# Kernel optimization log

Measured on AMD Instinct MI355X. Metric: run time of the kernel, lower is better.

Reference implementation:

```python
import jax, jax.numpy as jnp
import numpy as np

N = 100000
E = 1600000
IN_DIM = 128
OUT_DIM = 128


def setup_inputs() -> dict:
    key = jax.random.key(0)
    k1, k2, k3, k4, k5 = jax.random.split(key, 5)
    x = jax.random.normal(k1, (N, IN_DIM), dtype=jnp.float32)
    edge_index = jax.random.randint(k2, (2, E), 0, N, dtype=jnp.int64)
    # LayerNorm affine params
    ln_w = jnp.ones((IN_DIM,), dtype=jnp.float32)
    ln_b = jnp.zeros((IN_DIM,), dtype=jnp.float32)
    # SAGEConv params: lin_l (neighbor agg, with bias), lin_r (root, no bias)
    s = 1.0 / np.sqrt(IN_DIM)
    W_l = jax.random.uniform(k3, (OUT_DIM, IN_DIM), dtype=jnp.float32, minval=-s, maxval=s)
    b_l = jax.random.uniform(k4, (OUT_DIM,), dtype=jnp.float32, minval=-s, maxval=s)
    W_r = jax.random.uniform(k5, (OUT_DIM, IN_DIM), dtype=jnp.float32, minval=-s, maxval=s)
    return {"x": x, "edge_index": edge_index, "ln_w": ln_w, "ln_b": ln_b,
            "W_l": W_l, "b_l": b_l, "W_r": W_r}


def _layer_norm(x, w, b, eps=1e-5):
    mu = jnp.mean(x, axis=-1, keepdims=True)
    var = jnp.mean(jnp.square(x - mu), axis=-1, keepdims=True)
    return (x - mu) * jax.lax.rsqrt(var + eps) * w + b


def reference(x, edge_index, ln_w, ln_b, W_l, b_l, W_r):
    # norm -> activation -> dropout(p=0, identity)
    h = jax.nn.relu(_layer_norm(x, ln_w, ln_b))  # [N, in_dim]
    src = edge_index[0]  # message sources (x_j)
    dst = edge_index[1]  # aggregation targets
    # mean aggregation of neighbor features onto target nodes
    agg = jax.ops.segment_sum(h[src], dst, num_segments=N)  # [N, in_dim]
    cnt = jax.ops.segment_sum(jnp.ones((E,), dtype=h.dtype), dst, num_segments=N)
    agg = agg / jnp.maximum(cnt, 1.0)[:, None]
    # SAGEConv: lin_l(agg) + lin_r(h)
    out = agg @ W_l.T + b_l + h @ W_r.T  # [N, out_dim]
    return out
```

## Files before the change

kernel.cpp:

```cpp
#include <hip/hip_runtime.h>

#define N_NODES 100000
#define E_EDGES 1600000
#define DIM     128

#define NB1     196
#define CHUNK   8192
#define NBINS   512
#define NBUCKET 391
#define NBH     (NBINS * NB1)
#define HS_BLOCKS 98

#define HB_OFF    0
#define WTB_OFF   25600000
#define OFFS_OFF  25665536
#define BH_OFF    26065600
#define BSUM_OFF  26467008
#define BIN_OFF   26468032
#define SRC_OFF   32868032

typedef __attribute__((ext_vector_type(8))) short short8;
typedef __attribute__((ext_vector_type(4))) float floatx4;

__device__ __forceinline__ unsigned bf16pack(float a, float b) {
  unsigned ua = __float_as_uint(a); ua += 0x7fffu + ((ua >> 16) & 1u);
  unsigned ub = __float_as_uint(b); ub += 0x7fffu + ((ub >> 16) & 1u);
  return (ua >> 16) | (ub & 0xffff0000u);
}
__device__ __forceinline__ float2 bf16unpack(unsigned p) {
  return make_float2(__uint_as_float(p << 16), __uint_as_float(p & 0xffff0000u));
}

__global__ __launch_bounds__(256) void k_prep(const float* __restrict__ x,
                                              const float* __restrict__ lw,
                                              const float* __restrict__ lb,
                                              const float* __restrict__ Wl,
                                              const float* __restrict__ Wr,
                                              const int* __restrict__ ei,
                                              unsigned* __restrict__ hb,
                                              unsigned* __restrict__ wtb,
                                              int* __restrict__ bh) {
  int gid = blockIdx.x * 256 + threadIdx.x;
  int t = threadIdx.x;

  {
    int row  = blockIdx.x * 4 + (t >> 6);
    int lane = t & 63;
    float2 v = ((const float2*)(x + (size_t)row * DIM))[lane];
    float s  = v.x + v.y;
    float sq = v.x * v.x + v.y * v.y;
    #pragma unroll
    for (int off = 32; off > 0; off >>= 1) {
      s  += __shfl_xor(s, off);
      sq += __shfl_xor(sq, off);
    }
    float mu  = s * (1.0f / 128.0f);
    float var = sq * (1.0f / 128.0f) - mu * mu;
    float rs  = rsqrtf(var + 1e-5f);
    float2 w = ((const float2*)lw)[lane];
    float2 b = ((const float2*)lb)[lane];
    float ox = fmaxf((v.x - mu) * rs * w.x + b.x, 0.0f);
    float oy = fmaxf((v.y - mu) * rs * w.y + b.y, 0.0f);
    hb[(size_t)row * 64 + lane] = bf16pack(ox, oy);
  }

  if (gid < 16384) {
    int j2 = gid & 3;
    int q  = (gid >> 2) & 3;
    int c  = (gid >> 4) & 127;
    int kb = gid >> 11;
    int k0 = kb * 32 + q * 8 + j2 * 2;
    int k1 = k0 + 1;
    float v0 = (k0 < 128) ? Wl[c * 128 + k0] : Wr[c * 128 + (k0 - 128)];
    float v1 = (k1 < 128) ? Wl[c * 128 + k1] : Wr[c * 128 + (k1 - 128)];
    wtb[gid] = bf16pack(v0, v1);
  }

  if (blockIdx.x < NB1) {
    __shared__ int h[NBINS];
    h[t] = 0; h[t + 256] = 0;
    __syncthreads();
    const int4* d4p = (const int4*)(ei + E_EDGES);
    #pragma unroll
    for (int u = 0; u < 8; ++u) {
      int i4 = blockIdx.x * (CHUNK / 4) + u * 256 + t;
      if (i4 < E_EDGES / 4) {
        int4 d = d4p[i4];
        atomicAdd(&h[d.x >> 8], 1);
        atomicAdd(&h[d.y >> 8], 1);
        atomicAdd(&h[d.z >> 8], 1);
        atomicAdd(&h[d.w >> 8], 1);
      }
    }
    __syncthreads();
    bh[t * NB1 + blockIdx.x] = h[t];
    bh[(t + 256) * NB1 + blockIdx.x] = h[t + 256];
  }
}

__global__ __launch_bounds__(256) void k_hscan1(int* __restrict__ bh,
                                                int* __restrict__ bsum) {
  __shared__ int s[256];
  int t = threadIdx.x;
  int base = blockIdx.x * 1024 + t * 4;
  int a0 = (base + 0 < NBH) ? bh[base + 0] : 0;
  int a1 = (base + 1 < NBH) ? bh[base + 1] : 0;
  int a2 = (base + 2 < NBH) ? bh[base + 2] : 0;
  int a3 = (base + 3 < NBH) ? bh[base + 3] : 0;
  s[t] = a0 + a1 + a2 + a3;
  __syncthreads();
  #pragma unroll
  for (int off = 1; off < 256; off <<= 1) {
    int x = (t >= off) ? s[t - off] : 0;
    __syncthreads();
    s[t] += x;
    __syncthreads();
  }
  int excl = (t > 0) ? s[t - 1] : 0;
  if (t == 255) bsum[blockIdx.x] = s[255];
  if (base + 0 < NBH) bh[base + 0] = excl;
  if (base + 1 < NBH) bh[base + 1] = excl + a0;
  if (base + 2 < NBH) bh[base + 2] = excl + a0 + a1;
  if (base + 3 < NBH) bh[base + 3] = excl + a0 + a1 + a2;
}

__global__ __launch_bounds__(256) void k_binsort(const int* __restrict__ ei,
                                                 const int* __restrict__ bh,
                                                 const int* __restrict__ bsum,
                                                 int* __restrict__ binned) {
  __shared__ int stage[CHUNK];
  __shared__ int addr[CHUNK];
  __shared__ int hist[NBINS];
  __shared__ int ebase[NBINS];
  __shared__ int cur[NBINS];
  __shared__ int gbase[NBINS];
  __shared__ int s[256];
  __shared__ int bsc[256];
  int t  = threadIdx.x;
  int ch = blockIdx.x;

  s[t] = (t < HS_BLOCKS) ? bsum[t] : 0;
  __syncthreads();
  #pragma unroll
  for (int off = 1; off < 256; off <<= 1) {
    int xv = (t >= off) ? s[t - off] : 0;
    __syncthreads();
    s[t] += xv;
    __syncthreads();
  }
  bsc[t] = (t > 0) ? s[t - 1] : 0;
  __syncthreads();

  {
    int i0 = t * NB1 + ch;
    int i1 = (t + 256) * NB1 + ch;
    gbase[t]       = bh[i0] + bsc[i0 >> 10];
    gbase[t + 256] = bh[i1] + bsc[i1 >> 10];
  }
  hist[t] = 0; hist[t + 256] = 0;
  __syncthreads();

  const int4* s4p = (const int4*)ei;
  const int4* d4p = (const int4*)(ei + E_EDGES);

  #pragma unroll
  for (int u = 0; u < 8; ++u) {
    int i4 = ch * (CHUNK / 4) + u * 256 + t;
    if (i4 < E_EDGES / 4) {
      int4 d = d4p[i4];
      atomicAdd(&hist[d.x >> 8], 1);
      atomicAdd(&hist[d.y >> 8], 1);
      atomicAdd(&hist[d.z >> 8], 1);
      atomicAdd(&hist[d.w >> 8], 1);
    }
  }
  __syncthreads();

  int h0 = hist[2 * t], h1 = hist[2 * t + 1];
  s[t] = h0 + h1;
  __syncthreads();
  #pragma unroll
  for (int off = 1; off < 256; off <<= 1) {
    int xv = (t >= off) ? s[t - off] : 0;
    __syncthreads();
    s[t] += xv;
    __syncthreads();
  }
  int ex = (t > 0) ? s[t - 1] : 0;
  ebase[2 * t] = ex;
  ebase[2 * t + 1] = ex + h0;
  cur[2 * t] = ex;
  cur[2 * t + 1] = ex + h0;
  __syncthreads();

  #pragma unroll
  for (int u = 0; u < 8; ++u) {
    int i4 = ch * (CHUNK / 4) + u * 256 + t;
    if (i4 < E_EDGES / 4) {
      int4 sv = s4p[i4];
      int4 dv = d4p[i4];
      {
        int bin = dv.x >> 8; int pos = atomicAdd(&cur[bin], 1);
        stage[pos] = sv.x | ((dv.x & 255) << 20);
        addr[pos]  = gbase[bin] + (pos - ebase[bin]);
      }
      {
        int bin = dv.y >> 8; int pos = atomicAdd(&cur[bin], 1);
        stage[pos] = sv.y | ((dv.y & 255) << 20);
        addr[pos]  = gbase[bin] + (pos - ebase[bin]);
      }
      {
        int bin = dv.z >> 8; int pos = atomicAdd(&cur[bin], 1);
        stage[pos] = sv.z | ((dv.z & 255) << 20);
        addr[pos]  = gbase[bin] + (pos - ebase[bin]);
      }
      {
        int bin = dv.w >> 8; int pos = atomicAdd(&cur[bin], 1);
        stage[pos] = sv.w | ((dv.w & 255) << 20);
        addr[pos]  = gbase[bin] + (pos - ebase[bin]);
      }
    }
  }
  __syncthreads();

  int cbase = ch * CHUNK;
  int cnt = E_EDGES - cbase;
  if (cnt > CHUNK) cnt = CHUNK;
  for (int i = t; i < cnt; i += 256)
    binned[addr[i]] = stage[i];
}

__global__ __launch_bounds__(256) void k_csr(const int* __restrict__ bh,
                                             const int* __restrict__ bsum,
                                             const int* __restrict__ binned,
                                             int* __restrict__ offs,
                                             int* __restrict__ srcidx) {
  __shared__ int h[256];
  __shared__ int s[256];
  __shared__ int cur[256];
  __shared__ int bsc[256];
  int t = threadIdx.x;
  int bin = blockIdx.x;

  s[t] = (t < HS_BLOCKS) ? bsum[t] : 0;
  __syncthreads();
  #pragma unroll
  for (int off = 1; off < 256; off <<= 1) {
    int xv = (t >= off) ? s[t - off] : 0;
    __syncthreads();
    s[t] += xv;
    __syncthreads();
  }
  bsc[t] = (t > 0) ? s[t - 1] : 0;
  __syncthreads();

  int i0 = bin * NB1, i1 = (bin + 1) * NB1;
  int base = bh[i0] + bsc[i0 >> 10];
  int end  = bh[i1] + bsc[i1 >> 10];

  h[t] = 0;
  __syncthreads();
  for (int i = base + t; i < end; i += 256)
    atomicAdd(&h[(binned[i] >> 20) & 255], 1);
  __syncthreads();
  s[t] = h[t];
  __syncthreads();
  #pragma unroll
  for (int off = 1; off < 256; off <<= 1) {
    int x = (t >= off) ? s[t - off] : 0;
    __syncthreads();
    s[t] += x;
    __syncthreads();
  }
  int excl = (t > 0) ? s[t - 1] : 0;
  cur[t] = excl;
  int node = bin * 256 + t;
  if (node < N_NODES) offs[node] = base + excl;
  if (node == N_NODES) offs[N_NODES] = E_EDGES;
  __syncthreads();
  for (int i = base + t; i < end; i += 256) {
    int p = binned[i];
    int r = atomicAdd(&cur[(p >> 20) & 255], 1);
    srcidx[base + r] = p & 0xFFFFF;
  }
}

__global__ __launch_bounds__(256) void k_gathgemm(const unsigned* __restrict__ hb,
                                                  const int* __restrict__ offs,
                                                  const int* __restrict__ srcidx,
                                                  const unsigned* __restrict__ wtb,
                                                  const float* __restrict__ bl,
                                                  float* __restrict__ out) {
  __shared__ unsigned agg[4][16 * 68];
  int wv   = threadIdx.x >> 6;
  int lane = threadIdx.x & 63;
  unsigned* ag = agg[wv];
  int r0w = (blockIdx.x * 4 + wv) * 16;

  for (int p = 0; p < 8; ++p) {
    int n0 = r0w + 2 * p;
    int n1 = n0 + 1;
    int c0 = (n0 < N_NODES) ? n0 : N_NODES;
    int c1 = (n0 + 1 < N_NODES) ? n0 + 1 : N_NODES;
    int c2 = (n1 + 1 < N_NODES) ? n1 + 1 : N_NODES;
    int b0 = __builtin_amdgcn_readfirstlane(offs[c0]);
    int e0 = __builtin_amdgcn_readfirstlane(offs[c1]);
    int b1 = e0;
    int e1 = __builtin_amdgcn_readfirstlane(offs[c2]);
    if (n1 > N_NODES) { b1 = e1 = b0; }
    int m0 = e0 - b0, m1 = e1 - b1;
    int c  = (m0 < m1 ? m0 : m1) & ~7;

    float ax0 = 0.0f, ay0 = 0.0f, ax1 = 0.0f, ay1 = 0.0f;

    for (int j = 0; j < c; j += 8) {
      unsigned p0[8], p1[8];
      #pragma unroll
      for (int i = 0; i < 8; ++i) {
        int s0 = srcidx[b0 + j + i];
        int s1 = srcidx[b1 + j + i];
        p0[i] = hb[(size_t)s0 * 64 + lane];
        p1[i] = hb[(size_t)s1 * 64 + lane];
      }
      #pragma unroll
      for (int i = 0; i < 8; ++i) {
        float2 v0 = bf16unpack(p0[i]);
        float2 v1 = bf16unpack(p1[i]);
        ax0 += v0.x; ay0 += v0.y;
        ax1 += v1.x; ay1 += v1.y;
      }
    }
    for (int j = b0 + c; j < e0; ) {
      int rem = e0 - j;
      if (rem >= 8) {
        unsigned pp[8];
        #pragma unroll
        for (int i = 0; i < 8; ++i) pp[i] = hb[(size_t)srcidx[j + i] * 64 + lane];
        #pragma unroll
        for (int i = 0; i < 8; ++i) { float2 v = bf16unpack(pp[i]); ax0 += v.x; ay0 += v.y; }
        j += 8;
      } else {
        float2 v = bf16unpack(hb[(size_t)srcidx[j] * 64 + lane]);
        ax0 += v.x; ay0 += v.y;
        ++j;
      }
    }
    for (int j = b1 + c; j < e1; ) {
      int rem = e1 - j;
      if (rem >= 8) {
        unsigned pp[8];
        #pragma unroll
        for (int i = 0; i < 8; ++i) pp[i] = hb[(size_t)srcidx[j + i] * 64 + lane];
        #pragma unroll
        for (int i = 0; i < 8; ++i) { float2 v = bf16unpack(pp[i]); ax1 += v.x; ay1 += v.y; }
        j += 8;
      } else {
        float2 v = bf16unpack(hb[(size_t)srcidx[j] * 64 + lane]);
        ax1 += v.x; ay1 += v.y;
        ++j;
      }
    }

    float inv0 = 1.0f / fmaxf((float)m0, 1.0f);
    float inv1 = 1.0f / fmaxf((float)m1, 1.0f);
    ag[(2 * p + 0) * 68 + lane] = bf16pack(ax0 * inv0, ay0 * inv0);
    ag[(2 * p + 1) * 68 + lane] = bf16pack(ax1 * inv1, ay1 * inv1);
  }

  int m = lane & 15;
  int q = lane >> 4;
  int rowA = r0w + m;
  if (rowA > N_NODES - 1) rowA = N_NODES - 1;

  short8 afrag[8];
  #pragma unroll
  for (int kb = 0; kb < 4; ++kb) {
    uint4 u = *(const uint4*)&ag[m * 68 + (kb * 4 + q) * 4];
    afrag[kb] = *(short8*)&u;
  }
  const uint4* hr = (const uint4*)(hb + (size_t)rowA * 64);
  #pragma unroll
  for (int kb = 0; kb < 4; ++kb) {
    uint4 u = hr[kb * 4 + q];
    afrag[kb + 4] = *(short8*)&u;
  }

  const uint4* b4 = (const uint4*)wtb;
  #pragma unroll
  for (int ct = 0; ct < 8; ++ct) {
    int col = ct * 16 + m;
    floatx4 acc = {0.0f, 0.0f, 0.0f, 0.0f};
    #pragma unroll
    for (int kb = 0; kb < 8; ++kb) {
      uint4 u = b4[kb * 512 + col * 4 + q];
      short8 bfrag = *(short8*)&u;
      acc = __builtin_amdgcn_mfma_f32_16x16x32_bf16(afrag[kb], bfrag, acc, 0, 0, 0);
    }
    float bias = bl[col];
    #pragma unroll
    for (int reg = 0; reg < 4; ++reg) {
      int r = r0w + q * 4 + reg;
      if (r < N_NODES) out[(size_t)r * DIM + col] = acc[reg] + bias;
    }
  }
}

extern "C" void kernel_launch(void* const* d_in, const int* in_sizes, int n_in,
                              void* d_out, int out_size, void* d_ws, size_t ws_size,
                              hipStream_t stream) {
  const float* x  = (const float*)d_in[0];
  const int*   ei = (const int*)d_in[1];
  const float* lw = (const float*)d_in[2];
  const float* lb = (const float*)d_in[3];
  const float* Wl = (const float*)d_in[4];
  const float* bl = (const float*)d_in[5];
  const float* Wr = (const float*)d_in[6];
  float* out = (float*)d_out;

  char* ws = (char*)d_ws;
  unsigned* hb     = (unsigned*)(ws + HB_OFF);
  unsigned* wtb    = (unsigned*)(ws + WTB_OFF);
  int*      offs   = (int*)(ws + OFFS_OFF);
  int*      bh     = (int*)(ws + BH_OFF);
  int*      bsum   = (int*)(ws + BSUM_OFF);
  int*      binned = (int*)(ws + BIN_OFF);
  int*      srcidx = (int*)(ws + SRC_OFF);

  k_prep<<<N_NODES / 4, 256, 0, stream>>>(x, lw, lb, Wl, Wr, ei, hb, wtb, bh);
  k_hscan1<<<HS_BLOCKS, 256, 0, stream>>>(bh, bsum);
  k_binsort<<<NB1, 256, 0, stream>>>(ei, bh, bsum, binned);
  k_csr<<<NBUCKET, 256, 0, stream>>>(bh, bsum, binned, offs, srcidx);
  k_gathgemm<<<(N_NODES + 63) / 64, 256, 0, stream>>>(hb, offs, srcidx, wtb, bl, out);
}
```

Before: 285.9 us.

## Split fused gather+GEMM into separate gather and GEMM kernels

Splits the fused gather-then-MFMA kernel into two kernels. The new gather kernel handles two nodes per wave across N/8 blocks, which gives far more parallelism than the old 16-rows-per-wave loop, and writes the bf16 mean aggregate to a global buffer. A separate GEMM kernel reads that buffer back. This trades an extra global write and read of about 25MB plus a kernel launch for better latency hiding in the gather.

```diff
diff --git a/kernel.cpp b/kernel.cpp
--- a/kernel.cpp
+++ b/kernel.cpp
@@ -18,6 +18,7 @@
 #define BSUM_OFF  26467008
 #define BIN_OFF   26468032
 #define SRC_OFF   32868032
+#define AGGB_OFF  39268032
 
 typedef __attribute__((ext_vector_type(8))) short short8;
 typedef __attribute__((ext_vector_type(4))) float floatx4;
@@ -285,100 +286,98 @@
   }
 }
 
-__global__ __launch_bounds__(256) void k_gathgemm(const unsigned* __restrict__ hb,
-                                                  const int* __restrict__ offs,
-                                                  const int* __restrict__ srcidx,
-                                                  const unsigned* __restrict__ wtb,
-                                                  const float* __restrict__ bl,
-                                                  float* __restrict__ out) {
-  __shared__ unsigned agg[4][16 * 68];
-  int wv   = threadIdx.x >> 6;
+__global__ __launch_bounds__(256) void k_gather(const unsigned* __restrict__ hb,
+                                                const int* __restrict__ offs,
+                                                const int* __restrict__ srcidx,
+                                                unsigned* __restrict__ aggb) {
+  int wave = threadIdx.x >> 6;
   int lane = threadIdx.x & 63;
-  unsigned* ag = agg[wv];
-  int r0w = (blockIdx.x * 4 + wv) * 16;
-
-  for (int p = 0; p < 8; ++p) {
-    int n0 = r0w + 2 * p;
-    int n1 = n0 + 1;
-    int c0 = (n0 < N_NODES) ? n0 : N_NODES;
-    int c1 = (n0 + 1 < N_NODES) ? n0 + 1 : N_NODES;
-    int c2 = (n1 + 1 < N_NODES) ? n1 + 1 : N_NODES;
-    int b0 = __builtin_amdgcn_readfirstlane(offs[c0]);
-    int e0 = __builtin_amdgcn_readfirstlane(offs[c1]);
-    int b1 = e0;
-    int e1 = __builtin_amdgcn_readfirstlane(offs[c2]);
-    if (n1 > N_NODES) { b1 = e1 = b0; }
-    int m0 = e0 - b0, m1 = e1 - b1;
-    int c  = (m0 < m1 ? m0 : m1) & ~7;
-
-    float ax0 = 0.0f, ay0 = 0.0f, ax1 = 0.0f, ay1 = 0.0f;
-
-    for (int j = 0; j < c; j += 8) {
-      unsigned p0[8], p1[8];
+  int n0 = blockIdx.x * 8 + wave * 2;
+  int n1 = n0 + 1;
+  int b0 = __builtin_amdgcn_readfirstlane(offs[n0]);
+  int e0 = __builtin_amdgcn_readfirstlane(offs[n0 + 1]);
+  int b1 = __builtin_amdgcn_readfirstlane(offs[n1]);
+  int e1 = __builtin_amdgcn_readfirstlane(offs[n1 + 1]);
+  int m0 = e0 - b0, m1 = e1 - b1;
+  int c  = (m0 < m1 ? m0 : m1) & ~7;
+
+  float ax0 = 0.0f, ay0 = 0.0f, ax1 = 0.0f, ay1 = 0.0f;
+
+  for (int j = 0; j < c; j += 8) {
+    unsigned p0[8], p1[8];
+    #pragma unroll
+    for (int i = 0; i < 8; ++i) {
+      int s0 = srcidx[b0 + j + i];
+      int s1 = srcidx[b1 + j + i];
+      p0[i] = hb[(size_t)s0 * 64 + lane];
+      p1[i] = hb[(size_t)s1 * 64 + lane];
+    }
+    #pragma unroll
+    for (int i = 0; i < 8; ++i) {
+      float2 v0 = bf16unpack(p0[i]);
+      float2 v1 = bf16unpack(p1[i]);
+      ax0 += v0.x; ay0 += v0.y;
+      ax1 += v1.x; ay1 += v1.y;
+    }
+  }
+  for (int j = b0 + c; j < e0; ) {
+    int rem = e0 - j;
+    if (rem >= 8) {
+      unsigned p[8];
       #pragma unroll
-      for (int i = 0; i < 8; ++i) {
-        int s0 = srcidx[b0 + j + i];
-        int s1 = srcidx[b1 + j + i];
-        p0[i] = hb[(size_t)s0 * 64 + lane];
-        p1[i] = hb[(size_t)s1 * 64 + lane];
-      }
+      for (int i = 0; i < 8; ++i) p[i] = hb[(size_t)srcidx[j + i] * 64 + lane];
       #pragma unroll
-      for (int i = 0; i < 8; ++i) {
-        float2 v0 = bf16unpack(p0[i]);
-        float2 v1 = bf16unpack(p1[i]);
-        ax0 += v0.x; ay0 += v0.y;
-        ax1 += v1.x; ay1 += v1.y;
-      }
-    }
-    for (int j = b0 + c; j < e0; ) {
-      int rem = e0 - j;
-      if (rem >= 8) {
-        unsigned pp[8];
-        #pragma unroll
-        for (int i = 0; i < 8; ++i) pp[i] = hb[(size_t)srcidx[j + i] * 64 + lane];
-        #pragma unroll
-        for (int i = 0; i < 8; ++i) { float2 v = bf16unpack(pp[i]); ax0 += v.x; ay0 += v.y; }
-        j += 8;
-      } else {
-        float2 v = bf16unpack(hb[(size_t)srcidx[j] * 64 + lane]);
-        ax0 += v.x; ay0 += v.y;
-        ++j;
-      }
-    }
-    for (int j = b1 + c; j < e1; ) {
-      int rem = e1 - j;
-      if (rem >= 8) {
-        unsigned pp[8];
-        #pragma unroll
-        for (int i = 0; i < 8; ++i) pp[i] = hb[(size_t)srcidx[j + i] * 64 + lane];
-        #pragma unroll
-        for (int i = 0; i < 8; ++i) { float2 v = bf16unpack(pp[i]); ax1 += v.x; ay1 += v.y; }
-        j += 8;
-      } else {
-        float2 v = bf16unpack(hb[(size_t)srcidx[j] * 64 + lane]);
-        ax1 += v.x; ay1 += v.y;
-        ++j;
-      }
-    }
-
-    float inv0 = 1.0f / fmaxf((float)m0, 1.0f);
-    float inv1 = 1.0f / fmaxf((float)m1, 1.0f);
-    ag[(2 * p + 0) * 68 + lane] = bf16pack(ax0 * inv0, ay0 * inv0);
-    ag[(2 * p + 1) * 68 + lane] = bf16pack(ax1 * inv1, ay1 * inv1);
-  }
-
+      for (int i = 0; i < 8; ++i) { float2 v = bf16unpack(p[i]); ax0 += v.x; ay0 += v.y; }
+      j += 8;
+    } else {
+      float2 v = bf16unpack(hb[(size_t)srcidx[j] * 64 + lane]);
+      ax0 += v.x; ay0 += v.y;
+      ++j;
+    }
+  }
+  for (int j = b1 + c; j < e1; ) {
+    int rem = e1 - j;
+    if (rem >= 8) {
+      unsigned p[8];
+      #pragma unroll
+      for (int i = 0; i < 8; ++i) p[i] = hb[(size_t)srcidx[j + i] * 64 + lane];
+      #pragma unroll
+      for (int i = 0; i < 8; ++i) { float2 v = bf16unpack(p[i]); ax1 += v.x; ay1 += v.y; }
+      j += 8;
+    } else {
+      float2 v = bf16unpack(hb[(size_t)srcidx[j] * 64 + lane]);
+      ax1 += v.x; ay1 += v.y;
+      ++j;
+    }
+  }
+
+  float inv0 = 1.0f / fmaxf((float)m0, 1.0f);
+  float inv1 = 1.0f / fmaxf((float)m1, 1.0f);
+  aggb[(size_t)n0 * 64 + lane] = bf16pack(ax0 * inv0, ay0 * inv0);
+  aggb[(size_t)n1 * 64 + lane] = bf16pack(ax1 * inv1, ay1 * inv1);
+}
+
+__global__ __launch_bounds__(256) void k_gemm(const unsigned* __restrict__ aggb,
+                                              const unsigned* __restrict__ hb,
+                                              const unsigned* __restrict__ wtb,
+                                              const float* __restrict__ bl,
+                                              float* __restrict__ out) {
+  int wave = threadIdx.x >> 6;
+  int lane = threadIdx.x & 63;
   int m = lane & 15;
   int q = lane >> 4;
-  int rowA = r0w + m;
+  int r0 = blockIdx.x * 64 + wave * 16;
+  int rowA = r0 + m;
   if (rowA > N_NODES - 1) rowA = N_NODES - 1;
 
+  const uint4* ar = (const uint4*)(aggb + (size_t)rowA * 64);
+  const uint4* hr = (const uint4*)(hb + (size_t)rowA * 64);
   short8 afrag[8];
   #pragma unroll
   for (int kb = 0; kb < 4; ++kb) {
-    uint4 u = *(const uint4*)&ag[m * 68 + (kb * 4 + q) * 4];
+    uint4 u = ar[kb * 4 + q];
     afrag[kb] = *(short8*)&u;
   }
-  const uint4* hr = (const uint4*)(hb + (size_t)rowA * 64);
   #pragma unroll
   for (int kb = 0; kb < 4; ++kb) {
     uint4 u = hr[kb * 4 + q];
@@ -388,19 +387,19 @@
   const uint4* b4 = (const uint4*)wtb;
   #pragma unroll
   for (int ct = 0; ct < 8; ++ct) {
-    int col = ct * 16 + m;
+    int c = ct * 16 + m;
     floatx4 acc = {0.0f, 0.0f, 0.0f, 0.0f};
     #pragma unroll
     for (int kb = 0; kb < 8; ++kb) {
-      uint4 u = b4[kb * 512 + col * 4 + q];
+      uint4 u = b4[kb * 512 + c * 4 + q];
       short8 bfrag = *(short8*)&u;
       acc = __builtin_amdgcn_mfma_f32_16x16x32_bf16(afrag[kb], bfrag, acc, 0, 0, 0);
     }
-    float bias = bl[col];
+    float bias = bl[c];
     #pragma unroll
     for (int reg = 0; reg < 4; ++reg) {
-      int r = r0w + q * 4 + reg;
-      if (r < N_NODES) out[(size_t)r * DIM + col] = acc[reg] + bias;
+      int r = r0 + q * 4 + reg;
+      if (r < N_NODES) out[(size_t)r * DIM + c] = acc[reg] + bias;
     }
   }
 }
@@ -425,10 +424,12 @@
   int*      bsum   = (int*)(ws + BSUM_OFF);
   int*      binned = (int*)(ws + BIN_OFF);
   int*      srcidx = (int*)(ws + SRC_OFF);
+  unsigned* aggb   = (unsigned*)(ws + AGGB_OFF);
 
   k_prep<<<N_NODES / 4, 256, 0, stream>>>(x, lw, lb, Wl, Wr, ei, hb, wtb, bh);
   k_hscan1<<<HS_BLOCKS, 256, 0, stream>>>(bh, bsum);
   k_binsort<<<NB1, 256, 0, stream>>>(ei, bh, bsum, binned);
   k_csr<<<NBUCKET, 256, 0, stream>>>(bh, bsum, binned, offs, srcidx);
-  k_gathgemm<<<(N_NODES + 63) / 64, 256, 0, stream>>>(hb, offs, srcidx, wtb, bl, out);
-}
+  k_gather<<<N_NODES / 8, 256, 0, stream>>>(hb, offs, srcidx, aggb);
+  k_gemm<<<(N_NODES + 63) / 64, 256, 0, stream>>>(aggb, hb, wtb, bl, out);
+}
```

Result: faster. 255.5 us (-10.6%).
